# Kernel tuning notes

Measured on AMD Instinct MI355X. Metric: run time of the kernel, lower is better.

## Reference

```python
import jax, jax.numpy as jnp
import numpy as np

NUM_HEADS = 8
FREQ_RATIO = 0.5


def _resize_bilinear(img, out_h, out_w):
    """Bilinear resize of last two dims, matching torch interpolate align_corners=False."""
    in_h, in_w = img.shape[-2], img.shape[-1]

    def idx(in_size, out_size):
        src = jnp.maximum((jnp.arange(out_size, dtype=jnp.float32) + 0.5) * (in_size / out_size) - 0.5, 0.0)
        i0 = jnp.floor(src).astype(jnp.int32)
        i1 = jnp.minimum(i0 + 1, in_size - 1)
        w = src - i0.astype(jnp.float32)
        return i0, i1, w

    r0, r1, wr = idx(in_h, out_h)
    img = img[..., r0, :] * (1.0 - wr)[:, None] + img[..., r1, :] * wr[:, None]
    c0, c1, wc = idx(in_w, out_w)
    img = img[..., c0] * (1.0 - wc) + img[..., c1] * wc
    return img


def setup_inputs() -> dict:
    key = jax.random.key(0)
    ks = jax.random.split(key, 6)
    B, T, J, C = 4, 256, 17, 512
    H = NUM_HEADS
    x = jax.random.normal(ks[0], (B, T, J, C), dtype=jnp.float32)
    att_map = jax.random.uniform(ks[1], (B, H, J, T, T), dtype=jnp.float32)
    weight = jax.random.uniform(ks[2], (1,), dtype=jnp.float32)
    w_qkv = jax.random.normal(ks[3], (C, 3 * C), dtype=jnp.float32) * 0.02
    w_proj = jax.random.normal(ks[4], (C, C), dtype=jnp.float32) * 0.02
    b_proj = jnp.zeros((C,), dtype=jnp.float32)
    freq_gate = jnp.ones((1,), dtype=jnp.float32)
    return {"x": x, "att_map": att_map, "weight": weight, "w_qkv": w_qkv,
            "w_proj": w_proj, "b_proj": b_proj, "freq_gate": freq_gate}


def reference(x, att_map, weight, w_qkv, w_proj, b_proj, freq_gate):
    B, T, J, C = x.shape
    H = NUM_HEADS
    d = C // H
    scale = d ** (-0.5)

    qkv = (x @ w_qkv).reshape(B, T, J, 3, H, d)
    qkv = jnp.transpose(qkv, (3, 0, 4, 2, 1, 5))  # [3,B,H,J,T,d]
    q, k, v = qkv[0], qkv[1], qkv[2]

    # time-domain attention over T, per (B,H,J)
    attn_time = jax.nn.softmax(jnp.einsum('bhjtd,bhjsd->bhjts', q, k) * scale, axis=-1)

    # frequency-domain attention
    qf = jnp.fft.rfft(q, axis=3)
    kf = jnp.fft.rfft(k, axis=3)
    F = qf.shape[3]                      # T//2 + 1
    keep = max(1, int(F * FREQ_RATIO))
    qf = qf[:, :, :, :keep]
    kf = kf[:, :, :, :keep]
    af = jnp.einsum('bhjfd,bhjgd->bhjfg', qf, jnp.conj(kf)) * scale  # complex [B,H,J,keep,keep]
    # torch combines softmax(real) + 1j*softmax(imag); only the real part survives
    af_real = jax.nn.softmax(af.real, axis=-1)
    af_real = jnp.pad(af_real, ((0, 0), (0, 0), (0, 0), (0, F - keep), (0, 0)))  # zero-pad rows to F
    attn_freq = _resize_bilinear(af_real, T, T)  # [B,H,J,T,T]

    gate = jax.nn.sigmoid(freq_gate)  # broadcastable scalar
    attn_self = gate * attn_freq + (1.0 - gate) * attn_time
    attn = weight * attn_self + (1.0 - weight) * att_map

    out = jnp.einsum('bhjts,bhjsd->bhjtd', attn, v)        # [B,H,J,T,d]
    out = jnp.transpose(out, (0, 3, 2, 1, 4)).reshape(B, T, J, C)
    return out @ w_proj + b_proj
```

## Files before the change

kernel.cpp:

```cpp
#include <hip/hip_runtime.h>
#include <hip/hip_bf16.h>


#define SCALE 0.125f
#define LSTR 72

typedef __attribute__((ext_vector_type(4))) float f32x4;
typedef __attribute__((ext_vector_type(8))) short bf16x8;
typedef __attribute__((ext_vector_type(8))) unsigned short u16x8;

__device__ __forceinline__ float bf2f(unsigned short u) {
  return __uint_as_float(((unsigned int)u) << 16);
}
__device__ __forceinline__ unsigned short f2bf(float f) {
  unsigned int u = __float_as_uint(f);
  u += 0x7FFFu + ((u >> 16) & 1u);
  return (unsigned short)(u >> 16);
}

__global__ __launch_bounds__(256) void conv_x(
    const float* __restrict__ x, unsigned short* __restrict__ xh,
    unsigned short* __restrict__ xl) {
  const size_t i = ((size_t)blockIdx.x * 256 + threadIdx.x) * 8;
  float4 a = *(const float4*)(x + i);
  float4 b = *(const float4*)(x + i + 4);
  float vv[8] = {a.x, a.y, a.z, a.w, b.x, b.y, b.z, b.w};
  u16x8 hi, lo;
#pragma unroll
  for (int e = 0; e < 8; ++e) {
    unsigned short h = f2bf(vv[e]);
    hi[e] = h;
    lo[e] = f2bf(vv[e] - bf2f(h));
  }
  *(u16x8*)&xh[i] = hi;
  *(u16x8*)&xl[i] = lo;
}

__global__ __launch_bounds__(256) void conv_wT(
    const float* __restrict__ w, unsigned short* __restrict__ th,
    unsigned short* __restrict__ tl, int N) {
  __shared__ float T[64][65];
  const int tid = threadIdx.x;
  const int nt = blockIdx.x * 64, kt = blockIdx.y * 64;
  for (int i = tid; i < 4096; i += 256) {
    const int r = i >> 6, c = i & 63;
    T[r][c] = w[(size_t)(kt + r) * N + nt + c];
  }
  __syncthreads();
  for (int i = tid; i < 4096; i += 256) {
    const int rn = i >> 6, ck = i & 63;
    const float v = T[ck][rn];
    const unsigned short h = f2bf(v);
    const size_t o = (size_t)(nt + rn) * 512 + kt + ck;
    th[o] = h;
    tl[o] = f2bf(v - bf2f(h));
  }
}

__global__ __launch_bounds__(256, 2) void qkv_gemm(
    const unsigned short* __restrict__ xh, const unsigned short* __restrict__ xl,
    const unsigned short* __restrict__ wh, const unsigned short* __restrict__ wl,
    float* __restrict__ q, float* __restrict__ k, float* __restrict__ v) {
  __shared__ __attribute__((aligned(16))) unsigned short Wt[2][128 * LSTR];
  __shared__ __attribute__((aligned(16))) unsigned short Xt[2][128 * LSTR];

  const int tid = threadIdx.x;
  const int bx = blockIdx.x, by = blockIdx.y;
  const int wid = tid >> 6, lane = tid & 63;
  const int lr = lane & 15, lg = lane >> 4;
  const int wr = wid >> 1, wc = wid & 1;
  const int srow = tid >> 3, skg = tid & 7;

  const unsigned short* xhp = xh + (size_t)(by * 128 + srow) * 512 + skg * 8;
  const unsigned short* xlp = xl + (size_t)(by * 128 + srow) * 512 + skg * 8;
  const unsigned short* whp = wh + (size_t)(bx * 128 + srow) * 512 + skg * 8;
  const unsigned short* wlp = wl + (size_t)(bx * 128 + srow) * 512 + skg * 8;

  u16x8 rxh[4], rxl[4], rwh[4], rwl[4];
  auto loadk = [&](int k0) {
#pragma unroll
    for (int it = 0; it < 4; ++it) {
      const size_t o = (size_t)(32 * it) * 512 + k0;
      rxh[it] = *(const u16x8*)(xhp + o);
      rxl[it] = *(const u16x8*)(xlp + o);
      rwh[it] = *(const u16x8*)(whp + o);
      rwl[it] = *(const u16x8*)(wlp + o);
    }
  };

  f32x4 acc[4][4];
#pragma unroll
  for (int nt = 0; nt < 4; ++nt)
#pragma unroll
    for (int mt = 0; mt < 4; ++mt) acc[nt][mt] = (f32x4){0.f, 0.f, 0.f, 0.f};

  loadk(0);
  for (int s = 0; s < 8; ++s) {
    if (s) __syncthreads();
#pragma unroll
    for (int it = 0; it < 4; ++it) {
      const int base = (srow + 32 * it) * LSTR + skg * 8;
      *(u16x8*)&Xt[0][base] = rxh[it];
      *(u16x8*)&Xt[1][base] = rxl[it];
      *(u16x8*)&Wt[0][base] = rwh[it];
      *(u16x8*)&Wt[1][base] = rwl[it];
    }
    __syncthreads();
    if (s < 7) loadk((s + 1) * 64);
#pragma unroll
    for (int kh = 0; kh < 2; ++kh) {
      const int kbase = kh * 32 + lg * 8;
      bf16x8 Ah[4], Al[4], Bh[4], Bl[4];
#pragma unroll
      for (int nt = 0; nt < 4; ++nt) {
        const int n = wr * 64 + nt * 16 + lr;
        Ah[nt] = *(bf16x8*)&Wt[0][n * LSTR + kbase];
        Al[nt] = *(bf16x8*)&Wt[1][n * LSTR + kbase];
      }
#pragma unroll
      for (int mt = 0; mt < 4; ++mt) {
        const int m = wc * 64 + mt * 16 + lr;
        Bh[mt] = *(bf16x8*)&Xt[0][m * LSTR + kbase];
        Bl[mt] = *(bf16x8*)&Xt[1][m * LSTR + kbase];
      }
#pragma unroll
      for (int nt = 0; nt < 4; ++nt)
#pragma unroll
        for (int mt = 0; mt < 4; ++mt) {
          acc[nt][mt] = __builtin_amdgcn_mfma_f32_16x16x32_bf16(Ah[nt], Bh[mt], acc[nt][mt], 0, 0, 0);
          acc[nt][mt] = __builtin_amdgcn_mfma_f32_16x16x32_bf16(Ah[nt], Bl[mt], acc[nt][mt], 0, 0, 0);
          acc[nt][mt] = __builtin_amdgcn_mfma_f32_16x16x32_bf16(Al[nt], Bh[mt], acc[nt][mt], 0, 0, 0);
        }
    }
  }

#pragma unroll
  for (int mt = 0; mt < 4; ++mt) {
    const int m = by * 128 + wc * 64 + mt * 16 + lr;
    const int jj = m % 17;
    const int bt = m / 17;
    const int t = bt & 255;
    const int b = bt >> 8;
#pragma unroll
    for (int nt = 0; nt < 4; ++nt) {
      const int c = bx * 128 + wr * 64 + nt * 16 + lg * 4;
      const int qi = c >> 9;
      const int h = (c >> 6) & 7;
      const int dd = c & 63;
      float* dst = (qi == 0) ? q : (qi == 1) ? k : v;
      *(float4*)&dst[((size_t)((b * 8 + h) * 17 + jj)) * 16384 + t * 64 + dd] =
          make_float4(acc[nt][mt][0], acc[nt][mt][1], acc[nt][mt][2], acc[nt][mt][3]);
    }
  }
}

__global__ __launch_bounds__(256) void freq_kernel(
    const float* __restrict__ qg, const float* __restrict__ kg,
    float* __restrict__ af_out) {
  __shared__ __attribute__((aligned(16))) unsigned short qT[2][64 * 256];
  __shared__ __attribute__((aligned(16))) unsigned short QF[4][64 * 64];
  __shared__ __attribute__((aligned(16))) unsigned short KF[4][64 * 64];

  const int tid = threadIdx.x;
  const int head = blockIdx.x;
  const int w = tid >> 6, lane = tid & 63;
  const int lr = lane & 15, lg = lane >> 4;
  const int f0 = w << 4;

  bf16x8 Ech[8], Ecl[8], Esh[8], Esl[8];
  {
    const int f = f0 + lr;
#pragma unroll
    for (int kb = 0; kb < 8; ++kb) {
      bf16x8 ch, cl, sh, sl;
#pragma unroll
      for (int i = 0; i < 8; ++i) {
        int t = kb * 32 + lg * 8 + i;
        int idx = (f * t) & 255;
        float s, c;
        __sincosf((float)idx * 0.02454369260617026f, &s, &c);
        unsigned short chh = f2bf(c);
        unsigned short shh = f2bf(s);
        ch[i] = (short)chh;
        cl[i] = (short)f2bf(c - bf2f(chh));
        sh[i] = (short)shh;
        sl[i] = (short)f2bf(s - bf2f(shh));
      }
      Ech[kb] = ch; Ecl[kb] = cl; Esh[kb] = sh; Esl[kb] = sl;
    }
  }

  for (int pass = 0; pass < 2; ++pass) {
    const float* src = pass ? kg : qg;
    __syncthreads();
    const float4* s4 = (const float4*)(src + head * 16384);
    for (int i = tid; i < 4096; i += 256) {
      int t = i >> 4, dq = i & 15;
      float4 v4 = s4[i];
      float vv[4] = {v4.x, v4.y, v4.z, v4.w};
#pragma unroll
      for (int c = 0; c < 4; ++c) {
        int d = dq * 4 + c;
        unsigned short hi = f2bf(vv[c]);
        unsigned short lo = f2bf(vv[c] - bf2f(hi));
        int byo = d * 512 + ((t * 2) ^ ((d & 31) << 4));
        *(unsigned short*)((char*)qT[0] + byo) = hi;
        *(unsigned short*)((char*)qT[1] + byo) = lo;
      }
    }
    __syncthreads();

    f32x4 ar[4], ai[4];
#pragma unroll
    for (int nt = 0; nt < 4; ++nt) {
      ar[nt] = (f32x4){0.f, 0.f, 0.f, 0.f};
      ai[nt] = (f32x4){0.f, 0.f, 0.f, 0.f};
    }
#pragma unroll
    for (int kb = 0; kb < 8; ++kb) {
#pragma unroll
      for (int nt = 0; nt < 4; ++nt) {
        const int d = nt * 16 + lr;
        const int byo = d * 512 + ((kb * 64 + lg * 16) ^ ((d & 31) << 4));
        bf16x8 bh = *(bf16x8*)((char*)qT[0] + byo);
        bf16x8 bl = *(bf16x8*)((char*)qT[1] + byo);
        ar[nt] = __builtin_amdgcn_mfma_f32_16x16x32_bf16(Ech[kb], bh, ar[nt], 0, 0, 0);
        ar[nt] = __builtin_amdgcn_mfma_f32_16x16x32_bf16(Ech[kb], bl, ar[nt], 0, 0, 0);
        ar[nt] = __builtin_amdgcn_mfma_f32_16x16x32_bf16(Ecl[kb], bh, ar[nt], 0, 0, 0);
        ai[nt] = __builtin_amdgcn_mfma_f32_16x16x32_bf16(Esh[kb], bh, ai[nt], 0, 0, 0);
        ai[nt] = __builtin_amdgcn_mfma_f32_16x16x32_bf16(Esh[kb], bl, ai[nt], 0, 0, 0);
        ai[nt] = __builtin_amdgcn_mfma_f32_16x16x32_bf16(Esl[kb], bh, ai[nt], 0, 0, 0);
      }
    }
    unsigned short(*DST)[64 * 64] = pass ? KF : QF;
#pragma unroll
    for (int nt = 0; nt < 4; ++nt) {
#pragma unroll
      for (int j = 0; j < 4; ++j) {
        const int f = f0 + lg * 4 + j;
        const int d = nt * 16 + lr;
        const int byo = f * 128 + ((d * 2) ^ ((f & 7) << 4));
        float vr = ar[nt][j], vi = ai[nt][j];
        unsigned short rh = f2bf(vr);
        unsigned short ih = f2bf(vi);
        *(unsigned short*)((char*)DST[0] + byo) = rh;
        *(unsigned short*)((char*)DST[1] + byo) = f2bf(vr - bf2f(rh));
        *(unsigned short*)((char*)DST[2] + byo) = ih;
        *(unsigned short*)((char*)DST[3] + byo) = f2bf(vi - bf2f(ih));
      }
    }
  }
  __syncthreads();

  f32x4 acc[4];
#pragma unroll
  for (int nt = 0; nt < 4; ++nt) acc[nt] = (f32x4){0.f, 0.f, 0.f, 0.f};
#pragma unroll
  for (int kb = 0; kb < 2; ++kb) {
    const int fA = f0 + lr;
    const int abyo = fA * 128 + ((kb * 64 + lg * 16) ^ ((fA & 7) << 4));
    bf16x8 arh = *(bf16x8*)((char*)QF[0] + abyo);
    bf16x8 arl = *(bf16x8*)((char*)QF[1] + abyo);
    bf16x8 aih = *(bf16x8*)((char*)QF[2] + abyo);
    bf16x8 ail = *(bf16x8*)((char*)QF[3] + abyo);
#pragma unroll
    for (int nt = 0; nt < 4; ++nt) {
      const int g = nt * 16 + lr;
      const int bbyo = g * 128 + ((kb * 64 + lg * 16) ^ ((g & 7) << 4));
      bf16x8 brh = *(bf16x8*)((char*)KF[0] + bbyo);
      bf16x8 brl = *(bf16x8*)((char*)KF[1] + bbyo);
      bf16x8 bih = *(bf16x8*)((char*)KF[2] + bbyo);
      bf16x8 bil = *(bf16x8*)((char*)KF[3] + bbyo);
      acc[nt] = __builtin_amdgcn_mfma_f32_16x16x32_bf16(arh, brh, acc[nt], 0, 0, 0);
      acc[nt] = __builtin_amdgcn_mfma_f32_16x16x32_bf16(arh, brl, acc[nt], 0, 0, 0);
      acc[nt] = __builtin_amdgcn_mfma_f32_16x16x32_bf16(arl, brh, acc[nt], 0, 0, 0);
      acc[nt] = __builtin_amdgcn_mfma_f32_16x16x32_bf16(aih, bih, acc[nt], 0, 0, 0);
      acc[nt] = __builtin_amdgcn_mfma_f32_16x16x32_bf16(aih, bil, acc[nt], 0, 0, 0);
      acc[nt] = __builtin_amdgcn_mfma_f32_16x16x32_bf16(ail, bih, acc[nt], 0, 0, 0);
    }
  }

  float* outh = af_out + head * 4096;
#pragma unroll
  for (int j = 0; j < 4; ++j) {
    float m = fmaxf(fmaxf(acc[0][j], acc[1][j]), fmaxf(acc[2][j], acc[3][j]));
#pragma unroll
    for (int mask = 1; mask < 16; mask <<= 1) m = fmaxf(m, __shfl_xor(m, mask));
    float e[4];
    float rs = 0.f;
#pragma unroll
    for (int nt = 0; nt < 4; ++nt) {
      e[nt] = __expf((acc[nt][j] - m) * SCALE);
      rs += e[nt];
    }
#pragma unroll
    for (int mask = 1; mask < 16; mask <<= 1) rs += __shfl_xor(rs, mask);
    const float inv = 1.0f / rs;
    const int f = f0 + lg * 4 + j;
#pragma unroll
    for (int nt = 0; nt < 4; ++nt) outh[f * 64 + nt * 16 + lr] = e[nt] * inv;
  }
}

__global__ __launch_bounds__(256) void attn_kernel(
    const float* __restrict__ qg, const float* __restrict__ kg,
    const float* __restrict__ vg, const float* __restrict__ af,
    const float* __restrict__ att_map, const float* __restrict__ weight,
    const float* __restrict__ fgate, float* __restrict__ out_perm) {
  __shared__ unsigned short Ks[256 * 64];
  __shared__ unsigned short Vt[64 * 256];
  __shared__ unsigned short afl[64 * 66];
  __shared__ unsigned short Psc[4][16 * 40];

  const int tid = threadIdx.x;
  const int t0 = blockIdx.x << 6;
  const int head = blockIdx.y;
  const int jj = head % 17;
  const int hb = head / 17;
  const int h = hb & 7;
  const int b = hb >> 3;

  const float4* ksrc = (const float4*)(kg + head * 16384);
  const float4* vsrc = (const float4*)(vg + head * 16384);
  for (int i = tid; i < 4096; i += 256) {
    int s = i >> 4, dq = i & 15;
    float4 kf = ksrc[i];
    ushort4 k4 = make_ushort4(f2bf(kf.x), f2bf(kf.y), f2bf(kf.z), f2bf(kf.w));
    int koff = s * 128 + ((dq * 8) ^ ((s & 7) << 4));
    *(ushort4*)((char*)Ks + koff) = k4;
    float4 vf = vsrc[i];
    float vv[4] = {vf.x, vf.y, vf.z, vf.w};
#pragma unroll
    for (int c = 0; c < 4; ++c) {
      int d = dq * 4 + c;
      int voff = d * 512 + ((s * 2) ^ ((d & 7) << 4));
      *(unsigned short*)((char*)Vt + voff) = f2bf(vv[c]);
    }
  }
  const float4* asrc = (const float4*)(af + head * 4096);
  for (int i = tid; i < 1024; i += 256) {
    float4 a4 = asrc[i];
    int f = i >> 4, gq = (i & 15) << 2;
    ushort4 a4b = make_ushort4(f2bf(a4.x), f2bf(a4.y), f2bf(a4.z), f2bf(a4.w));
    *(ushort4*)&afl[f * 66 + gq] = a4b;
  }
  __syncthreads();

  const int w = tid >> 6, lane = tid & 63;
  const int lr = lane & 15, lg = lane >> 4;
  const int tw = t0 + w * 16;

  bf16x8 aq[2];
  {
    const float* qrow = qg + head * 16384 + (tw + lr) * 64 + lg * 8;
#pragma unroll
    for (int kc = 0; kc < 2; ++kc) {
      float4 q0 = *(const float4*)(qrow + kc * 32);
      float4 q1 = *(const float4*)(qrow + kc * 32 + 4);
      bf16x8 a;
      a[0] = (short)f2bf(q0.x); a[1] = (short)f2bf(q0.y);
      a[2] = (short)f2bf(q0.z); a[3] = (short)f2bf(q0.w);
      a[4] = (short)f2bf(q1.x); a[5] = (short)f2bf(q1.y);
      a[6] = (short)f2bf(q1.z); a[7] = (short)f2bf(q1.w);
      aq[kc] = a;
    }
  }

  f32x4 S[16];
#pragma unroll
  for (int nt = 0; nt < 16; ++nt) {
    f32x4 accv = {0.f, 0.f, 0.f, 0.f};
#pragma unroll
    for (int kc = 0; kc < 2; ++kc) {
      int srow = nt * 16 + lr;
      int d0 = kc * 32 + lg * 8;
      int off = srow * 128 + ((d0 * 2) ^ ((srow & 7) << 4));
      bf16x8 bk = *(bf16x8*)((char*)Ks + off);
      accv = __builtin_amdgcn_mfma_f32_16x16x32_bf16(aq[kc], bk, accv, 0, 0, 0);
    }
    S[nt] = accv;
  }

  float inv[4], mrow[4];
#pragma unroll
  for (int j = 0; j < 4; ++j) {
    float m = -1e30f;
#pragma unroll
    for (int nt = 0; nt < 16; ++nt) m = fmaxf(m, S[nt][j]);
#pragma unroll
    for (int mask = 1; mask < 16; mask <<= 1) m = fmaxf(m, __shfl_xor(m, mask));
    mrow[j] = m;
  }
#pragma unroll
  for (int j = 0; j < 4; ++j) {
    float rs = 0.f;
#pragma unroll
    for (int nt = 0; nt < 16; ++nt) {
      float e = __expf((S[nt][j] - mrow[j]) * SCALE);
      S[nt][j] = e;
      rs += e;
    }
#pragma unroll
    for (int mask = 1; mask < 16; mask <<= 1) rs += __shfl_xor(rs, mask);
    inv[j] = 1.0f / rs;
  }

  {
    const float wv = weight[0];
    const float gate = 1.0f / (1.0f + __expf(-fgate[0]));
    const float* amh = att_map + (size_t)head * 65536;
#pragma unroll
    for (int j = 0; j < 4; ++j) {
      const int t = tw + lg * 4 + j;
      float srcf = fmaxf((t + 0.5f) * (129.0f / 256.0f) - 0.5f, 0.0f);
      int f0r = (int)srcf;
      float wf = srcf - (float)f0r;
      int f1r = f0r + 1;
      if (f1r > 128) f1r = 128;
      const bool v0 = (f0r < 64), v1 = (f1r < 64);
#pragma unroll
      for (int nt = 0; nt < 16; ++nt) {
        const int s = nt * 16 + lr;
        float am = amh[t * 256 + s];
        float srcg = fmaxf((s + 0.5f) * 0.25f - 0.5f, 0.0f);
        int g0 = (int)srcg;
        float wc = srcg - (float)g0;
        int g1 = g0 + 1;
        if (g1 > 63) g1 = 63;
        float fr = 0.f;
        if (v0)
          fr += (1.0f - wf) *
                (bf2f(afl[f0r * 66 + g0]) * (1.0f - wc) + bf2f(afl[f0r * 66 + g1]) * wc);
        if (v1)
          fr += wf *
                (bf2f(afl[f1r * 66 + g0]) * (1.0f - wc) + bf2f(afl[f1r * 66 + g1]) * wc);
        float pt = S[nt][j] * inv[j];
        S[nt][j] = wv * (gate * fr + (1.0f - gate) * pt) + (1.0f - wv) * am;
      }
    }
  }

  f32x4 O[4];
#pragma unroll
  for (int dt = 0; dt < 4; ++dt) O[dt] = (f32x4){0.f, 0.f, 0.f, 0.f};
  unsigned short* psc = Psc[w];
#pragma unroll
  for (int sb = 0; sb < 8; ++sb) {
#pragma unroll
    for (int half = 0; half < 2; ++half) {
      const int nt = sb * 2 + half;
#pragma unroll
      for (int j = 0; j < 4; ++j) {
        psc[(lg * 4 + j) * 40 + half * 16 + lr] = f2bf(S[nt][j]);
      }
    }
    bf16x8 pa = *(bf16x8*)&psc[lr * 40 + lg * 8];
#pragma unroll
    for (int dt = 0; dt < 4; ++dt) {
      int d = dt * 16 + lr;
      int s0 = sb * 32 + lg * 8;
      int off = d * 512 + ((s0 * 2) ^ ((d & 7) << 4));
      bf16x8 bv = *(bf16x8*)((char*)Vt + off);
      O[dt] = __builtin_amdgcn_mfma_f32_16x16x32_bf16(pa, bv, O[dt], 0, 0, 0);
    }
  }

#pragma unroll
  for (int j = 0; j < 4; ++j) {
    const int t = tw + lg * 4 + j;
    float* orow = out_perm + ((size_t)((b * 256 + t) * 17 + jj)) * 512 + h * 64;
#pragma unroll
    for (int dt = 0; dt < 4; ++dt) {
      orow[dt * 16 + lr] = O[dt][j];
    }
  }
}

__global__ __launch_bounds__(256, 2) void proj_gemm(
    const float* __restrict__ A,
    const unsigned short* __restrict__ wh, const unsigned short* __restrict__ wl,
    const float* __restrict__ bias, float* __restrict__ out) {
  __shared__ __attribute__((aligned(16))) unsigned short Wt[2][128 * LSTR];
  __shared__ __attribute__((aligned(16))) unsigned short Xt[2][128 * LSTR];

  const int tid = threadIdx.x;
  const int bx = blockIdx.x, by = blockIdx.y;
  const int wid = tid >> 6, lane = tid & 63;
  const int lr = lane & 15, lg = lane >> 4;
  const int wr = wid >> 1, wc = wid & 1;
  const int srow = tid >> 3, skg = tid & 7;

  const float* ap = A + (size_t)(by * 128 + srow) * 512 + skg * 8;
  const unsigned short* whp = wh + (size_t)(bx * 128 + srow) * 512 + skg * 8;
  const unsigned short* wlp = wl + (size_t)(bx * 128 + srow) * 512 + skg * 8;

  float4 rA[4][2];
  u16x8 rwh[4], rwl[4];
  auto loadk = [&](int k0) {
#pragma unroll
    for (int it = 0; it < 4; ++it) {
      const size_t o = (size_t)(32 * it) * 512 + k0;
      rA[it][0] = *(const float4*)(ap + o);
      rA[it][1] = *(const float4*)(ap + o + 4);
      rwh[it] = *(const u16x8*)(whp + o);
      rwl[it] = *(const u16x8*)(wlp + o);
    }
  };

  f32x4 acc[4][4];
#pragma unroll
  for (int nt = 0; nt < 4; ++nt)
#pragma unroll
    for (int mt = 0; mt < 4; ++mt) acc[nt][mt] = (f32x4){0.f, 0.f, 0.f, 0.f};

  loadk(0);
  for (int s = 0; s < 8; ++s) {
    if (s) __syncthreads();
#pragma unroll
    for (int it = 0; it < 4; ++it) {
      const int base = (srow + 32 * it) * LSTR + skg * 8;
      float vv[8] = {rA[it][0].x, rA[it][0].y, rA[it][0].z, rA[it][0].w,
                     rA[it][1].x, rA[it][1].y, rA[it][1].z, rA[it][1].w};
      u16x8 hi, lo;
#pragma unroll
      for (int e = 0; e < 8; ++e) {
        unsigned short h = f2bf(vv[e]);
        hi[e] = h;
        lo[e] = f2bf(vv[e] - bf2f(h));
      }
      *(u16x8*)&Xt[0][base] = hi;
      *(u16x8*)&Xt[1][base] = lo;
      *(u16x8*)&Wt[0][base] = rwh[it];
      *(u16x8*)&Wt[1][base] = rwl[it];
    }
    __syncthreads();
    if (s < 7) loadk((s + 1) * 64);
#pragma unroll
    for (int kh = 0; kh < 2; ++kh) {
      const int kbase = kh * 32 + lg * 8;
      bf16x8 Ah[4], Al[4], Bh[4], Bl[4];
#pragma unroll
      for (int nt = 0; nt < 4; ++nt) {
        const int n = wr * 64 + nt * 16 + lr;
        Ah[nt] = *(bf16x8*)&Wt[0][n * LSTR + kbase];
        Al[nt] = *(bf16x8*)&Wt[1][n * LSTR + kbase];
      }
#pragma unroll
      for (int mt = 0; mt < 4; ++mt) {
        const int m = wc * 64 + mt * 16 + lr;
        Bh[mt] = *(bf16x8*)&Xt[0][m * LSTR + kbase];
        Bl[mt] = *(bf16x8*)&Xt[1][m * LSTR + kbase];
      }
#pragma unroll
      for (int nt = 0; nt < 4; ++nt)
#pragma unroll
        for (int mt = 0; mt < 4; ++mt) {
          acc[nt][mt] = __builtin_amdgcn_mfma_f32_16x16x32_bf16(Ah[nt], Bh[mt], acc[nt][mt], 0, 0, 0);
          acc[nt][mt] = __builtin_amdgcn_mfma_f32_16x16x32_bf16(Ah[nt], Bl[mt], acc[nt][mt], 0, 0, 0);
          acc[nt][mt] = __builtin_amdgcn_mfma_f32_16x16x32_bf16(Al[nt], Bh[mt], acc[nt][mt], 0, 0, 0);
        }
    }
  }

#pragma unroll
  for (int mt = 0; mt < 4; ++mt) {
    const int m = by * 128 + wc * 64 + mt * 16 + lr;
#pragma unroll
    for (int nt = 0; nt < 4; ++nt) {
      const int n = bx * 128 + wr * 64 + nt * 16 + lg * 4;
      float4 bi = *(const float4*)&bias[n];
      *(float4*)&out[(size_t)m * 512 + n] =
          make_float4(acc[nt][mt][0] + bi.x, acc[nt][mt][1] + bi.y,
                      acc[nt][mt][2] + bi.z, acc[nt][mt][3] + bi.w);
    }
  }
}

extern "C" void kernel_launch(void* const* d_in, const int* in_sizes, int n_in,
                              void* d_out, int out_size, void* d_ws, size_t ws_size,
                              hipStream_t stream) {
  (void)in_sizes; (void)n_in; (void)out_size; (void)ws_size;
  const float* x = (const float*)d_in[0];
  const float* att_map = (const float*)d_in[1];
  const float* weight = (const float*)d_in[2];
  const float* w_qkv = (const float*)d_in[3];
  const float* w_proj = (const float*)d_in[4];
  const float* b_proj = (const float*)d_in[5];
  const float* fgate = (const float*)d_in[6];
  float* out = (float*)d_out;

  char* ws = (char*)d_ws;
  const size_t HB = 35651584;
  const size_t AF = 8912896;
  float* qb = (float*)(ws);
  float* kb = (float*)(ws + HB);
  float* vb = (float*)(ws + 2 * HB);
  float* af = (float*)(ws + 3 * HB);
  char* base = ws + 3 * HB + AF;
  unsigned short* xh = (unsigned short*)(base);
  unsigned short* xl = (unsigned short*)(base + 17825792);
  float* out_perm = (float*)(base);
  unsigned short* wqh = (unsigned short*)(base + 35651584);
  unsigned short* wql = (unsigned short*)(base + 35651584 + 1572864);
  unsigned short* wph = (unsigned short*)(base + 35651584 + 2 * 1572864);
  unsigned short* wpl = (unsigned short*)(base + 35651584 + 2 * 1572864 + 524288);

  conv_x<<<4352, 256, 0, stream>>>(x, xh, xl);
  conv_wT<<<dim3(24, 8), 256, 0, stream>>>(w_qkv, wqh, wql, 1536);
  conv_wT<<<dim3(8, 8), 256, 0, stream>>>(w_proj, wph, wpl, 512);
  qkv_gemm<<<dim3(12, 136), 256, 0, stream>>>(xh, xl, wqh, wql, qb, kb, vb);
  freq_kernel<<<544, 256, 0, stream>>>(qb, kb, af);
  attn_kernel<<<dim3(4, 544), 256, 0, stream>>>(qb, kb, vb, af, att_map, weight,
                                                fgate, out_perm);
  proj_gemm<<<dim3(4, 136), 256, 0, stream>>>(out_perm, wph, wpl, b_proj, out);
}
```

Before: 412.7 us.

## Process all query rows per head in one block and prefetch att_map rows

The attention kernel now launches one block per (b,h,j) head instead of four, and each wave loops over four 16-row query tiles. This stops K/V/af from being loaded and converted to shared memory four times per head. The att_map tile for the next iteration is loaded into registers before the PV MFMA phase so its global latency overlaps compute, and launch bounds request two blocks per CU. The trade-offs are fewer blocks in the grid (544), more register pressure from the 64-float prefetch buffer, and a serial loop inside each block.

```diff
diff --git a/kernel.cpp b/kernel.cpp
--- a/kernel.cpp
+++ b/kernel.cpp
@@ -302,7 +302,7 @@
   }
 }
 
-__global__ __launch_bounds__(256) void attn_kernel(
+__global__ __launch_bounds__(256, 2) void attn_kernel(
     const float* __restrict__ qg, const float* __restrict__ kg,
     const float* __restrict__ vg, const float* __restrict__ af,
     const float* __restrict__ att_map, const float* __restrict__ weight,
@@ -313,12 +313,26 @@
   __shared__ unsigned short Psc[4][16 * 40];
 
   const int tid = threadIdx.x;
-  const int t0 = blockIdx.x << 6;
-  const int head = blockIdx.y;
+  const int head = blockIdx.x;
   const int jj = head % 17;
   const int hb = head / 17;
   const int h = hb & 7;
   const int b = hb >> 3;
+  const int w = tid >> 6, lane = tid & 63;
+  const int lr = lane & 15, lg = lane >> 4;
+
+  const float* amh = att_map + (size_t)head * 65536;
+
+  float amr[4][16];
+  {
+    const int tw = w * 64;
+#pragma unroll
+    for (int j = 0; j < 4; ++j) {
+      const float* rp = amh + (tw + lg * 4 + j) * 256 + lr;
+#pragma unroll
+      for (int nt = 0; nt < 16; ++nt) amr[j][nt] = rp[nt * 16];
+    }
+  }
 
   const float4* ksrc = (const float4*)(kg + head * 16384);
   const float4* vsrc = (const float4*)(vg + head * 16384);
@@ -346,69 +360,68 @@
   }
   __syncthreads();
 
-  const int w = tid >> 6, lane = tid & 63;
-  const int lr = lane & 15, lg = lane >> 4;
-  const int tw = t0 + w * 16;
-
-  bf16x8 aq[2];
-  {
-    const float* qrow = qg + head * 16384 + (tw + lr) * 64 + lg * 8;
-#pragma unroll
-    for (int kc = 0; kc < 2; ++kc) {
-      float4 q0 = *(const float4*)(qrow + kc * 32);
-      float4 q1 = *(const float4*)(qrow + kc * 32 + 4);
-      bf16x8 a;
-      a[0] = (short)f2bf(q0.x); a[1] = (short)f2bf(q0.y);
-      a[2] = (short)f2bf(q0.z); a[3] = (short)f2bf(q0.w);
-      a[4] = (short)f2bf(q1.x); a[5] = (short)f2bf(q1.y);
-      a[6] = (short)f2bf(q1.z); a[7] = (short)f2bf(q1.w);
-      aq[kc] = a;
-    }
-  }
-
-  f32x4 S[16];
-#pragma unroll
-  for (int nt = 0; nt < 16; ++nt) {
-    f32x4 accv = {0.f, 0.f, 0.f, 0.f};
-#pragma unroll
-    for (int kc = 0; kc < 2; ++kc) {
-      int srow = nt * 16 + lr;
-      int d0 = kc * 32 + lg * 8;
-      int off = srow * 128 + ((d0 * 2) ^ ((srow & 7) << 4));
-      bf16x8 bk = *(bf16x8*)((char*)Ks + off);
-      accv = __builtin_amdgcn_mfma_f32_16x16x32_bf16(aq[kc], bk, accv, 0, 0, 0);
-    }
-    S[nt] = accv;
-  }
-
-  float inv[4], mrow[4];
-#pragma unroll
-  for (int j = 0; j < 4; ++j) {
-    float m = -1e30f;
-#pragma unroll
-    for (int nt = 0; nt < 16; ++nt) m = fmaxf(m, S[nt][j]);
-#pragma unroll
-    for (int mask = 1; mask < 16; mask <<= 1) m = fmaxf(m, __shfl_xor(m, mask));
-    mrow[j] = m;
-  }
-#pragma unroll
-  for (int j = 0; j < 4; ++j) {
-    float rs = 0.f;
+  const float wv = weight[0];
+  const float gate = 1.0f / (1.0f + __expf(-fgate[0]));
+  unsigned short* psc = Psc[w];
+
+  for (int tt = 0; tt < 4; ++tt) {
+    const int tw = w * 64 + tt * 16;
+
+    bf16x8 aq[2];
+    {
+      const float* qrow = qg + head * 16384 + (tw + lr) * 64 + lg * 8;
+#pragma unroll
+      for (int kc = 0; kc < 2; ++kc) {
+        float4 q0 = *(const float4*)(qrow + kc * 32);
+        float4 q1 = *(const float4*)(qrow + kc * 32 + 4);
+        bf16x8 a;
+        a[0] = (short)f2bf(q0.x); a[1] = (short)f2bf(q0.y);
+        a[2] = (short)f2bf(q0.z); a[3] = (short)f2bf(q0.w);
+        a[4] = (short)f2bf(q1.x); a[5] = (short)f2bf(q1.y);
+        a[6] = (short)f2bf(q1.z); a[7] = (short)f2bf(q1.w);
+        aq[kc] = a;
+      }
+    }
+
+    f32x4 S[16];
 #pragma unroll
     for (int nt = 0; nt < 16; ++nt) {
-      float e = __expf((S[nt][j] - mrow[j]) * SCALE);
-      S[nt][j] = e;
-      rs += e;
-    }
-#pragma unroll
-    for (int mask = 1; mask < 16; mask <<= 1) rs += __shfl_xor(rs, mask);
-    inv[j] = 1.0f / rs;
-  }
-
-  {
-    const float wv = weight[0];
-    const float gate = 1.0f / (1.0f + __expf(-fgate[0]));
-    const float* amh = att_map + (size_t)head * 65536;
+      f32x4 accv = {0.f, 0.f, 0.f, 0.f};
+#pragma unroll
+      for (int kc = 0; kc < 2; ++kc) {
+        int srow = nt * 16 + lr;
+        int d0 = kc * 32 + lg * 8;
+        int off = srow * 128 + ((d0 * 2) ^ ((srow & 7) << 4));
+        bf16x8 bk = *(bf16x8*)((char*)Ks + off);
+        accv = __builtin_amdgcn_mfma_f32_16x16x32_bf16(aq[kc], bk, accv, 0, 0, 0);
+      }
+      S[nt] = accv;
+    }
+
+    float inv[4], mrow[4];
+#pragma unroll
+    for (int j = 0; j < 4; ++j) {
+      float m = -1e30f;
+#pragma unroll
+      for (int nt = 0; nt < 16; ++nt) m = fmaxf(m, S[nt][j]);
+#pragma unroll
+      for (int mask = 1; mask < 16; mask <<= 1) m = fmaxf(m, __shfl_xor(m, mask));
+      mrow[j] = m;
+    }
+#pragma unroll
+    for (int j = 0; j < 4; ++j) {
+      float rs = 0.f;
+#pragma unroll
+      for (int nt = 0; nt < 16; ++nt) {
+        float e = __expf((S[nt][j] - mrow[j]) * SCALE);
+        S[nt][j] = e;
+        rs += e;
+      }
+#pragma unroll
+      for (int mask = 1; mask < 16; mask <<= 1) rs += __shfl_xor(rs, mask);
+      inv[j] = 1.0f / rs;
+    }
+
 #pragma unroll
     for (int j = 0; j < 4; ++j) {
       const int t = tw + lg * 4 + j;
@@ -421,7 +434,7 @@
 #pragma unroll
       for (int nt = 0; nt < 16; ++nt) {
         const int s = nt * 16 + lr;
-        float am = amh[t * 256 + s];
+        float am = amr[j][nt];
         float srcg = fmaxf((s + 0.5f) * 0.25f - 0.5f, 0.0f);
         int g0 = (int)srcg;
         float wc = srcg - (float)g0;
@@ -438,40 +451,49 @@
         S[nt][j] = wv * (gate * fr + (1.0f - gate) * pt) + (1.0f - wv) * am;
       }
     }
-  }
-
-  f32x4 O[4];
-#pragma unroll
-  for (int dt = 0; dt < 4; ++dt) O[dt] = (f32x4){0.f, 0.f, 0.f, 0.f};
-  unsigned short* psc = Psc[w];
-#pragma unroll
-  for (int sb = 0; sb < 8; ++sb) {
-#pragma unroll
-    for (int half = 0; half < 2; ++half) {
-      const int nt = sb * 2 + half;
+
+    if (tt < 3) {
+      const int twn = w * 64 + (tt + 1) * 16;
 #pragma unroll
       for (int j = 0; j < 4; ++j) {
-        psc[(lg * 4 + j) * 40 + half * 16 + lr] = f2bf(S[nt][j]);
-      }
-    }
-    bf16x8 pa = *(bf16x8*)&psc[lr * 40 + lg * 8];
-#pragma unroll
-    for (int dt = 0; dt < 4; ++dt) {
-      int d = dt * 16 + lr;
-      int s0 = sb * 32 + lg * 8;
-      int off = d * 512 + ((s0 * 2) ^ ((d & 7) << 4));
-      bf16x8 bv = *(bf16x8*)((char*)Vt + off);
-      O[dt] = __builtin_amdgcn_mfma_f32_16x16x32_bf16(pa, bv, O[dt], 0, 0, 0);
-    }
-  }
-
-#pragma unroll
-  for (int j = 0; j < 4; ++j) {
-    const int t = tw + lg * 4 + j;
-    float* orow = out_perm + ((size_t)((b * 256 + t) * 17 + jj)) * 512 + h * 64;
-#pragma unroll
-    for (int dt = 0; dt < 4; ++dt) {
-      orow[dt * 16 + lr] = O[dt][j];
+        const float* rp = amh + (twn + lg * 4 + j) * 256 + lr;
+#pragma unroll
+        for (int nt = 0; nt < 16; ++nt) amr[j][nt] = rp[nt * 16];
+      }
+    }
+
+    f32x4 O[4];
+#pragma unroll
+    for (int dt = 0; dt < 4; ++dt) O[dt] = (f32x4){0.f, 0.f, 0.f, 0.f};
+#pragma unroll
+    for (int sb = 0; sb < 8; ++sb) {
+#pragma unroll
+      for (int half = 0; half < 2; ++half) {
+        const int nt = sb * 2 + half;
+#pragma unroll
+        for (int j = 0; j < 4; ++j) {
+          psc[(lg * 4 + j) * 40 + half * 16 + lr] = f2bf(S[nt][j]);
+        }
+      }
+      bf16x8 pa = *(bf16x8*)&psc[lr * 40 + lg * 8];
+#pragma unroll
+      for (int dt = 0; dt < 4; ++dt) {
+        int d = dt * 16 + lr;
+        int s0 = sb * 32 + lg * 8;
+        int off = d * 512 + ((s0 * 2) ^ ((d & 7) << 4));
+        bf16x8 bv = *(bf16x8*)((char*)Vt + off);
+        O[dt] = __builtin_amdgcn_mfma_f32_16x16x32_bf16(pa, bv, O[dt], 0, 0, 0);
+      }
+    }
+
+#pragma unroll
+    for (int j = 0; j < 4; ++j) {
+      const int t = tw + lg * 4 + j;
+      float* orow = out_perm + ((size_t)((b * 256 + t) * 17 + jj)) * 512 + h * 64;
+#pragma unroll
+      for (int dt = 0; dt < 4; ++dt) {
+        orow[dt * 16 + lr] = O[dt][j];
+      }
     }
   }
 }
@@ -610,7 +632,7 @@
   conv_wT<<<dim3(8, 8), 256, 0, stream>>>(w_proj, wph, wpl, 512);
   qkv_gemm<<<dim3(12, 136), 256, 0, stream>>>(xh, xl, wqh, wql, qb, kb, vb);
   freq_kernel<<<544, 256, 0, stream>>>(qb, kb, af);
-  attn_kernel<<<dim3(4, 544), 256, 0, stream>>>(qb, kb, vb, af, att_map, weight,
-                                                fgate, out_perm);
+  attn_kernel<<<544, 256, 0, stream>>>(qb, kb, vb, af, att_map, weight,
+                                       fgate, out_perm);
   proj_gemm<<<dim3(4, 136), 256, 0, stream>>>(out_perm, wph, wpl, b_proj, out);
 }
```

Result: slower. 574.5 us (+39.2%).

## Process all query tiles of a head in one block to reuse staged K/V

Applied to the files above, without the earlier changes.

The attention kernel now launches one block per (b,h,j) head instead of four, and each wave loops over four 16-row query tiles. K, V and the frequency map are converted and staged into shared memory once per head rather than four times, and the next Q tile is prefetched into registers while the current tile's softmax runs. This removes redundant global loads and bf16 conversions at the cost of fewer blocks (544 instead of 2176), less parallelism and a longer serial loop per block.

```diff
diff --git a/kernel.cpp b/kernel.cpp
--- a/kernel.cpp
+++ b/kernel.cpp
@@ -313,12 +313,26 @@
   __shared__ unsigned short Psc[4][16 * 40];
 
   const int tid = threadIdx.x;
-  const int t0 = blockIdx.x << 6;
-  const int head = blockIdx.y;
+  const int head = blockIdx.x;
   const int jj = head % 17;
   const int hb = head / 17;
   const int h = hb & 7;
   const int b = hb >> 3;
+  const int w = tid >> 6, lane = tid & 63;
+  const int lr = lane & 15, lg = lane >> 4;
+
+  const float* amh = att_map + (size_t)head * 65536;
+  const float* qbase = qg + head * 16384;
+
+  float4 rq[4];
+  {
+    const float* qrow = qbase + (w * 64 + lr) * 64 + lg * 8;
+#pragma unroll
+    for (int kc = 0; kc < 2; ++kc) {
+      rq[kc * 2 + 0] = *(const float4*)(qrow + kc * 32);
+      rq[kc * 2 + 1] = *(const float4*)(qrow + kc * 32 + 4);
+    }
+  }
 
   const float4* ksrc = (const float4*)(kg + head * 16384);
   const float4* vsrc = (const float4*)(vg + head * 16384);
@@ -346,17 +360,18 @@
   }
   __syncthreads();
 
-  const int w = tid >> 6, lane = tid & 63;
-  const int lr = lane & 15, lg = lane >> 4;
-  const int tw = t0 + w * 16;
-
-  bf16x8 aq[2];
-  {
-    const float* qrow = qg + head * 16384 + (tw + lr) * 64 + lg * 8;
+  const float wv = weight[0];
+  const float gate = 1.0f / (1.0f + __expf(-fgate[0]));
+  unsigned short* psc = Psc[w];
+
+  for (int tt = 0; tt < 4; ++tt) {
+    const int tw = w * 64 + tt * 16;
+
+    bf16x8 aq[2];
 #pragma unroll
     for (int kc = 0; kc < 2; ++kc) {
-      float4 q0 = *(const float4*)(qrow + kc * 32);
-      float4 q1 = *(const float4*)(qrow + kc * 32 + 4);
+      float4 q0 = rq[kc * 2 + 0];
+      float4 q1 = rq[kc * 2 + 1];
       bf16x8 a;
       a[0] = (short)f2bf(q0.x); a[1] = (short)f2bf(q0.y);
       a[2] = (short)f2bf(q0.z); a[3] = (short)f2bf(q0.w);
@@ -364,51 +379,55 @@
       a[6] = (short)f2bf(q1.z); a[7] = (short)f2bf(q1.w);
       aq[kc] = a;
     }
-  }
-
-  f32x4 S[16];
-#pragma unroll
-  for (int nt = 0; nt < 16; ++nt) {
-    f32x4 accv = {0.f, 0.f, 0.f, 0.f};
-#pragma unroll
-    for (int kc = 0; kc < 2; ++kc) {
-      int srow = nt * 16 + lr;
-      int d0 = kc * 32 + lg * 8;
-      int off = srow * 128 + ((d0 * 2) ^ ((srow & 7) << 4));
-      bf16x8 bk = *(bf16x8*)((char*)Ks + off);
-      accv = __builtin_amdgcn_mfma_f32_16x16x32_bf16(aq[kc], bk, accv, 0, 0, 0);
-    }
-    S[nt] = accv;
-  }
-
-  float inv[4], mrow[4];
-#pragma unroll
-  for (int j = 0; j < 4; ++j) {
-    float m = -1e30f;
-#pragma unroll
-    for (int nt = 0; nt < 16; ++nt) m = fmaxf(m, S[nt][j]);
-#pragma unroll
-    for (int mask = 1; mask < 16; mask <<= 1) m = fmaxf(m, __shfl_xor(m, mask));
-    mrow[j] = m;
-  }
-#pragma unroll
-  for (int j = 0; j < 4; ++j) {
-    float rs = 0.f;
+
+    f32x4 S[16];
 #pragma unroll
     for (int nt = 0; nt < 16; ++nt) {
-      float e = __expf((S[nt][j] - mrow[j]) * SCALE);
-      S[nt][j] = e;
-      rs += e;
-    }
-#pragma unroll
-    for (int mask = 1; mask < 16; mask <<= 1) rs += __shfl_xor(rs, mask);
-    inv[j] = 1.0f / rs;
-  }
-
-  {
-    const float wv = weight[0];
-    const float gate = 1.0f / (1.0f + __expf(-fgate[0]));
-    const float* amh = att_map + (size_t)head * 65536;
+      f32x4 accv = {0.f, 0.f, 0.f, 0.f};
+#pragma unroll
+      for (int kc = 0; kc < 2; ++kc) {
+        int srow = nt * 16 + lr;
+        int d0 = kc * 32 + lg * 8;
+        int off = srow * 128 + ((d0 * 2) ^ ((srow & 7) << 4));
+        bf16x8 bk = *(bf16x8*)((char*)Ks + off);
+        accv = __builtin_amdgcn_mfma_f32_16x16x32_bf16(aq[kc], bk, accv, 0, 0, 0);
+      }
+      S[nt] = accv;
+    }
+
+    if (tt < 3) {
+      const float* qrow = qbase + (tw + 16 + lr) * 64 + lg * 8;
+#pragma unroll
+      for (int kc = 0; kc < 2; ++kc) {
+        rq[kc * 2 + 0] = *(const float4*)(qrow + kc * 32);
+        rq[kc * 2 + 1] = *(const float4*)(qrow + kc * 32 + 4);
+      }
+    }
+
+    float inv[4], mrow[4];
+#pragma unroll
+    for (int j = 0; j < 4; ++j) {
+      float m = -1e30f;
+#pragma unroll
+      for (int nt = 0; nt < 16; ++nt) m = fmaxf(m, S[nt][j]);
+#pragma unroll
+      for (int mask = 1; mask < 16; mask <<= 1) m = fmaxf(m, __shfl_xor(m, mask));
+      mrow[j] = m;
+    }
+#pragma unroll
+    for (int j = 0; j < 4; ++j) {
+      float rs = 0.f;
+#pragma unroll
+      for (int nt = 0; nt < 16; ++nt) {
+        float e = __expf((S[nt][j] - mrow[j]) * SCALE);
+        S[nt][j] = e;
+        rs += e;
+      }
+#pragma unroll
+      for (int mask = 1; mask < 16; mask <<= 1) rs += __shfl_xor(rs, mask);
+      inv[j] = 1.0f / rs;
+    }
+
 #pragma unroll
     for (int j = 0; j < 4; ++j) {
       const int t = tw + lg * 4 + j;
@@ -438,40 +457,39 @@
         S[nt][j] = wv * (gate * fr + (1.0f - gate) * pt) + (1.0f - wv) * am;
       }
     }
-  }
-
-  f32x4 O[4];
-#pragma unroll
-  for (int dt = 0; dt < 4; ++dt) O[dt] = (f32x4){0.f, 0.f, 0.f, 0.f};
-  unsigned short* psc = Psc[w];
-#pragma unroll
-  for (int sb = 0; sb < 8; ++sb) {
-#pragma unroll
-    for (int half = 0; half < 2; ++half) {
-      const int nt = sb * 2 + half;
-#pragma unroll
-      for (int j = 0; j < 4; ++j) {
-        psc[(lg * 4 + j) * 40 + half * 16 + lr] = f2bf(S[nt][j]);
-      }
-    }
-    bf16x8 pa = *(bf16x8*)&psc[lr * 40 + lg * 8];
-#pragma unroll
-    for (int dt = 0; dt < 4; ++dt) {
-      int d = dt * 16 + lr;
-      int s0 = sb * 32 + lg * 8;
-      int off = d * 512 + ((s0 * 2) ^ ((d & 7) << 4));
-      bf16x8 bv = *(bf16x8*)((char*)Vt + off);
-      O[dt] = __builtin_amdgcn_mfma_f32_16x16x32_bf16(pa, bv, O[dt], 0, 0, 0);
-    }
-  }
-
-#pragma unroll
-  for (int j = 0; j < 4; ++j) {
-    const int t = tw + lg * 4 + j;
-    float* orow = out_perm + ((size_t)((b * 256 + t) * 17 + jj)) * 512 + h * 64;
-#pragma unroll
-    for (int dt = 0; dt < 4; ++dt) {
-      orow[dt * 16 + lr] = O[dt][j];
+
+    f32x4 O[4];
+#pragma unroll
+    for (int dt = 0; dt < 4; ++dt) O[dt] = (f32x4){0.f, 0.f, 0.f, 0.f};
+#pragma unroll
+    for (int sb = 0; sb < 8; ++sb) {
+#pragma unroll
+      for (int half = 0; half < 2; ++half) {
+        const int nt = sb * 2 + half;
+#pragma unroll
+        for (int j = 0; j < 4; ++j) {
+          psc[(lg * 4 + j) * 40 + half * 16 + lr] = f2bf(S[nt][j]);
+        }
+      }
+      bf16x8 pa = *(bf16x8*)&psc[lr * 40 + lg * 8];
+#pragma unroll
+      for (int dt = 0; dt < 4; ++dt) {
+        int d = dt * 16 + lr;
+        int s0 = sb * 32 + lg * 8;
+        int off = d * 512 + ((s0 * 2) ^ ((d & 7) << 4));
+        bf16x8 bv = *(bf16x8*)((char*)Vt + off);
+        O[dt] = __builtin_amdgcn_mfma_f32_16x16x32_bf16(pa, bv, O[dt], 0, 0, 0);
+      }
+    }
+
+#pragma unroll
+    for (int j = 0; j < 4; ++j) {
+      const int t = tw + lg * 4 + j;
+      float* orow = out_perm + ((size_t)((b * 256 + t) * 17 + jj)) * 512 + h * 64;
+#pragma unroll
+      for (int dt = 0; dt < 4; ++dt) {
+        orow[dt * 16 + lr] = O[dt][j];
+      }
     }
   }
 }
@@ -610,7 +628,7 @@
   conv_wT<<<dim3(8, 8), 256, 0, stream>>>(w_proj, wph, wpl, 512);
   qkv_gemm<<<dim3(12, 136), 256, 0, stream>>>(xh, xl, wqh, wql, qb, kb, vb);
   freq_kernel<<<544, 256, 0, stream>>>(qb, kb, af);
-  attn_kernel<<<dim3(4, 544), 256, 0, stream>>>(qb, kb, vb, af, att_map, weight,
-                                                fgate, out_perm);
+  attn_kernel<<<544, 256, 0, stream>>>(qb, kb, vb, af, att_map, weight,
+                                       fgate, out_perm);
   proj_gemm<<<dim3(4, 136), 256, 0, stream>>>(out_perm, wph, wpl, b_proj, out);
 }
```

Result: faster. 400.6 us (-2.9%).
